# Kernel optimization log

Hardware: AMD Instinct MI355X
Metric: run time of the kernel (lower is better)

## Reference

```python
import jax, jax.numpy as jnp
from jax import lax
import numpy as np

B, ENC, H, DE, T = 16384, 512, 256, 32, 64


def setup_inputs() -> dict:
    key = jax.random.key(0)
    ks = jax.random.split(key, 12)
    s = lambda fan: 1.0 / np.sqrt(fan)
    return {
        "encoded_input_series": jax.random.normal(ks[0], (B, ENC), jnp.float32),
        "final_x_val": jax.random.normal(ks[1], (B, 1), jnp.float32),
        # embed_func: Dense(DE) applied to scalar input (last dim = 1)
        "W_emb": jax.random.normal(ks[2], (1, DE), jnp.float32) * s(1),
        "b_emb": jnp.zeros((DE,), jnp.float32),
        # encode_reshape layer: Dense(H) on encoded series -> initial h
        "W_enc": jax.random.normal(ks[3], (ENC, H), jnp.float32) * s(ENC),
        "b_enc": jnp.zeros((H,), jnp.float32),
        # LSTM cell params (Keras gate order i, f, c, o)
        "W_k": jax.random.normal(ks[4], (DE, 4 * H), jnp.float32) * s(DE),
        "W_r": jax.random.normal(ks[5], (H, 4 * H), jnp.float32) * s(H),
        "b_lstm": jnp.concatenate([jnp.zeros((H,)), jnp.ones((H,)), jnp.zeros((2 * H,))]).astype(jnp.float32),
        # reduce layer: Dense(1)
        "W_red": jax.random.normal(ks[6], (H, 1), jnp.float32) * s(H),
        "b_red": jnp.zeros((1,), jnp.float32),
        "decode_length": T,
    }


def reference(encoded_input_series, final_x_val, W_emb, b_emb, W_enc, b_enc,
              W_k, W_r, b_lstm, W_red, b_red, decode_length):
    Hdim = W_r.shape[0]
    # initial hidden state from encoder summary; cell state zero-initialized
    h0 = encoded_input_series @ W_enc + b_enc            # [B, H]
    c0 = jnp.zeros_like(h0)
    # initial decoder input: embed of last observed value
    x0 = final_x_val @ W_emb + b_emb                     # [B, DE]

    def step(carry, _):
        h, c, x = carry
        gates = x @ W_k + h @ W_r + b_lstm               # [B, 4H]
        i, f, cb, o = jnp.split(gates, 4, axis=-1)
        c_new = jax.nn.sigmoid(f) * c + jax.nn.sigmoid(i) * jnp.tanh(cb)
        h_new = jax.nn.sigmoid(o) * jnp.tanh(c_new)
        y = h_new @ W_red + b_red                        # [B, 1]
        x_next = y @ W_emb + b_emb
        return (h_new, c_new, x_next), y[:, 0]

    _, ys = lax.scan(step, (h0, c0, x0), None, length=decode_length)
    return ys.T                                          # [B, T]
```

## Files before the change

kernel.cpp:

```cpp
#include <hip/hip_runtime.h>
#include <hip/hip_bf16.h>
#include <math.h>


typedef _Float16 f16x8 __attribute__((ext_vector_type(8)));
typedef float f32x4 __attribute__((ext_vector_type(4)));

#define DEV __device__ __forceinline__

constexpr int ENC = 512;
constexpr int HD  = 256;
constexpr int DE  = 32;
constexpr int TT  = 64;
constexpr int NG  = 4 * HD;
constexpr int NKT = 8;
constexpr int TS  = 528;
constexpr int BR  = 32;
constexpr int NMT = 2;

DEV bool is_f32(const void* blstm) {
  return ((const unsigned*)blstm)[256] == 0x3F800000u;
}
DEV float ldf(const void* p, size_t i, bool f32) {
  return f32 ? ((const float*)p)[i]
             : __bfloat162float(((const __hip_bfloat16*)p)[i]);
}
DEV void split2h(float v, _Float16& hi, _Float16& lo) {
  hi = (_Float16)v;
  lo = (_Float16)(v - (float)hi);
}
DEV void ld8cvt2h(const void* p, size_t i, bool f32, f16x8& hi, f16x8& lo) {
  if (f32) {
    const f32x4* q = (const f32x4*)((const float*)p + i);
    f32x4 u0 = q[0], u1 = q[1];
#pragma unroll
    for (int j = 0; j < 4; ++j) {
      float a = u0[j], b = u1[j];
      _Float16 ah = (_Float16)a, bh = (_Float16)b;
      hi[j] = ah; hi[4 + j] = bh;
      lo[j] = (_Float16)(a - (float)ah); lo[4 + j] = (_Float16)(b - (float)bh);
    }
  } else {
    const __hip_bfloat16* s = (const __hip_bfloat16*)p + i;
#pragma unroll
    for (int j = 0; j < 8; ++j) {
      float a = __bfloat162float(s[j]);
      _Float16 ah = (_Float16)a;
      hi[j] = ah;
      lo[j] = (_Float16)(a - (float)ah);
    }
  }
}
DEV f16x8 load8h(const _Float16* p) {
  return *reinterpret_cast<const f16x8*>(p);
}

constexpr float L2E = 1.44269504088896f;
DEV float sigm(float x) {
  return __builtin_amdgcn_rcpf(1.0f + __builtin_amdgcn_exp2f(-L2E * x));
}
DEV float tanh_(float x) {
  return 2.0f * __builtin_amdgcn_rcpf(1.0f + __builtin_amdgcn_exp2f(-2.0f * L2E * x)) - 1.0f;
}

__global__ __launch_bounds__(256) void pack_w(const void* __restrict__ wr,
                                              const void* __restrict__ bl,
                                              _Float16* __restrict__ dhi) {
  const bool f32 = is_f32(bl);
  int idx = blockIdx.x * 256 + threadIdx.x;
  if (idx >= NKT * 64 * 64) return;
  int lane = idx & 63, tile = idx >> 6;
  int nt = tile & 63, ks = tile >> 6;
  int kb = ks * 32 + ((lane >> 4) << 3);
  int n  = (nt << 4) + (lane & 15);
#pragma unroll
  for (int j = 0; j < 8; ++j)
    dhi[idx * 8 + j] = (_Float16)ldf(wr, (size_t)(kb + j) * NG + n, f32);
}

__global__ __launch_bounds__(256) void pack_e(const void* __restrict__ we,
                                              const void* __restrict__ bl,
                                              _Float16* __restrict__ dhi,
                                              _Float16* __restrict__ dlo) {
  const bool f32 = is_f32(bl);
  int idx = blockIdx.x * 256 + threadIdx.x;
  if (idx >= 16 * 16 * 64) return;
  int lane = idx & 63, tile = idx >> 6;
  int nt = tile & 15, ks = tile >> 4;
  int kb = ks * 32 + ((lane >> 4) << 3);
  int n  = (nt << 4) + (lane & 15);
#pragma unroll
  for (int j = 0; j < 8; ++j) {
    float v = ldf(we, (size_t)(kb + j) * HD + n, f32);
    _Float16 h, l;
    split2h(v, h, l);
    dhi[idx * 8 + j] = h;
    dlo[idx * 8 + j] = l;
  }
}

__global__ __launch_bounds__(256) void pack_vec(const void* __restrict__ wemb,
                                                const void* __restrict__ bemb,
                                                const void* __restrict__ wk,
                                                const void* __restrict__ bl,
                                                float* __restrict__ wk2,
                                                float* __restrict__ bp) {
  const bool f32 = is_f32(bl);
  int n = blockIdx.x * 256 + threadIdx.x;
  if (n >= NG) return;
  float s1 = 0.f, s2 = 0.f;
  for (int j = 0; j < DE; ++j) {
    float wkv = ldf(wk, (size_t)j * NG + n, f32);
    s1 += ldf(wemb, j, f32) * wkv;
    s2 += ldf(bemb, j, f32) * wkv;
  }
  wk2[n] = s1;
  bp[n]  = s2 + ldf(bl, n, f32);
}

__global__ __launch_bounds__(512)
__attribute__((amdgpu_waves_per_eu(4, 4)))
void lstm_main(
    const void* __restrict__ enc,
    const void* __restrict__ fx,
    const void* __restrict__ benc,
    const void* __restrict__ blstm,
    const void* __restrict__ wred,
    const void* __restrict__ bredp,
    const _Float16* __restrict__ pWhi,
    const _Float16* __restrict__ pEhi,
    const _Float16* __restrict__ pElo,
    const float* __restrict__ wk2,
    const float* __restrict__ bp,
    const int* __restrict__ dlen,
    void* __restrict__ out) {
  __shared__ __align__(16) _Float16 frag[2][NMT * NKT * TS];
  __shared__ __align__(16) float wredf[HD];
  __shared__ __align__(16) float bpL[NG];
  __shared__ __align__(16) float wk2L[NG];
  __shared__ __align__(16) float y_lds[BR];

  const bool f32 = is_f32(blstm);
  const int tid  = threadIdx.x;
  const int w    = tid >> 6;
  const int lane = tid & 63;
  const int q    = lane >> 4;
  const int cl   = lane & 15;
  const int r0   = blockIdx.x * BR;
  int Tn = dlen[0];
  if (Tn < 1 || Tn > TT) Tn = TT;

  const int aoff = lane * 8;
  const int hwb = w * TS + q * 32 + 128 * (cl >> 3) + (cl & 7);
  const int cbase = w * 32 + cl;

  const int yrow  = tid >> 4, ypart = tid & 15;
  const int ybase = ((yrow >> 4) * NKT + (ypart >> 1)) * TS +
                    ((yrow & 15) + 16 * ((ypart & 1) * 2)) * 8;

  if (tid < HD) wredf[tid] = ldf(wred, tid, f32);
  if (tid < BR) y_lds[tid] = ldf(fx, r0 + tid, f32);
  bpL[tid]        = bp[tid];
  bpL[tid + 512]  = bp[tid + 512];
  wk2L[tid]       = wk2[tid];
  wk2L[tid + 512] = wk2[tid + 512];
  const float bredf = ldf(bredp, 0, f32);

  f32x4 acc0[NMT][2];
  {
    float be0 = ldf(benc, w * 32 + cl, f32);
    float be1 = ldf(benc, w * 32 + 16 + cl, f32);
#pragma unroll
    for (int mt = 0; mt < NMT; ++mt) {
      acc0[mt][0] = (f32x4){be0, be0, be0, be0};
      acc0[mt][1] = (f32x4){be1, be1, be1, be1};
    }
  }
  const size_t ebase = ((size_t)(w * 2) * 64 + lane) * 8;
#pragma unroll 1
  for (int ks = 0; ks < ENC / 32; ++ks) {
    f16x8 bh[2], bl2[2];
#pragma unroll
    for (int hh = 0; hh < 2; ++hh) {
      size_t fo = ebase + (size_t)(ks * 16 + hh) * 512;
      bh[hh]  = load8h(pEhi + fo);
      bl2[hh] = load8h(pElo + fo);
    }
#pragma unroll
    for (int mt = 0; mt < NMT; ++mt) {
      f16x8 ah, al;
      ld8cvt2h(enc, (size_t)(r0 + mt * 16 + cl) * ENC + ks * 32 + q * 8, f32, ah, al);
#pragma unroll
      for (int hh = 0; hh < 2; ++hh) {
        acc0[mt][hh] = __builtin_amdgcn_mfma_f32_16x16x32_f16(ah, bh[hh],  acc0[mt][hh], 0, 0, 0);
        acc0[mt][hh] = __builtin_amdgcn_mfma_f32_16x16x32_f16(al, bh[hh],  acc0[mt][hh], 0, 0, 0);
        acc0[mt][hh] = __builtin_amdgcn_mfma_f32_16x16x32_f16(ah, bl2[hh], acc0[mt][hh], 0, 0, 0);
      }
    }
  }
#pragma unroll
  for (int mt = 0; mt < NMT; ++mt)
#pragma unroll
    for (int hh = 0; hh < 2; ++hh)
#pragma unroll
      for (int r = 0; r < 4; ++r) {
        int idx = mt * NKT * TS + hwb + r * 8 + hh * 256;
        frag[0][idx] = (_Float16)acc0[mt][hh][r];
      }

  f32x4 cst[NMT][2];
#pragma unroll
  for (int mt = 0; mt < NMT; ++mt)
#pragma unroll
    for (int hh = 0; hh < 2; ++hh) cst[mt][hh] = (f32x4){0.f, 0.f, 0.f, 0.f};

  __syncthreads();

  const _Float16* wbase = pWhi + ((size_t)(w * 2) * 64 + lane) * 8;

  int rb = 0;
#pragma unroll 1
  for (int t = 0; t < Tn; ++t) {
    const _Float16* FH = &frag[rb][0];
    _Float16* WH = &frag[rb ^ 1][0];

    f32x4 acc[NMT][8];
#pragma unroll
    for (int nf = 0; nf < 8; ++nf) {
      int col = (nf >> 1) * 256 + (nf & 1) * 16 + cbase;
      float bb = bpL[col];
#pragma unroll
      for (int mt = 0; mt < NMT; ++mt) acc[mt][nf] = (f32x4){bb, bb, bb, bb};
    }

#pragma unroll 1
    for (int j = 0; j < 8; ++j) {
      int ks = (j + w) & 7;
#pragma unroll
      for (int half = 0; half < 2; ++half) {
        f16x8 bc[4];
#pragma unroll
        for (int p = 0; p < 4; ++p)
          bc[p] = load8h(wbase +
                         (size_t)(ks * 64 + (half * 2 + (p >> 1)) * 16 + (p & 1)) * 512);
#pragma unroll
        for (int mt = 0; mt < NMT; ++mt) {
          f16x8 ah = load8h(&FH[(mt * NKT + ks) * TS + aoff]);
#pragma unroll
          for (int p = 0; p < 4; ++p)
            acc[mt][half * 4 + p] =
                __builtin_amdgcn_mfma_f32_16x16x32_f16(ah, bc[p], acc[mt][half * 4 + p], 0, 0, 0);
        }
      }
    }

    if (t > 0) {
      float sum = 0.f;
#pragma unroll
      for (int jj = 0; jj < 2; ++jj) {
        f16x8 hv = load8h(&FH[ybase + jj * 128]);
#pragma unroll
        for (int j = 0; j < 8; ++j)
          sum += (float)hv[j] * wredf[ypart * 16 + jj * 8 + j];
      }
      sum += __shfl_xor(sum, 1);
      sum += __shfl_xor(sum, 2);
      sum += __shfl_xor(sum, 4);
      sum += __shfl_xor(sum, 8);
      float y = sum + bredf;
      if (ypart == 0) {
        size_t oi = (size_t)(r0 + yrow) * TT + (t - 1);
        if (f32) ((float*)out)[oi] = y;
        else     ((__hip_bfloat16*)out)[oi] = __float2bfloat16(y);
        y_lds[yrow] = y;
      }
    }
    __syncthreads();

    f32x4 yv[NMT];
#pragma unroll
    for (int mt = 0; mt < NMT; ++mt)
      yv[mt] = *(const f32x4*)&y_lds[mt * 16 + q * 4];
#pragma unroll
    for (int nf = 0; nf < 8; ++nf) {
      int col = (nf >> 1) * 256 + (nf & 1) * 16 + cbase;
      float wv = wk2L[col];
#pragma unroll
      for (int mt = 0; mt < NMT; ++mt)
#pragma unroll
        for (int r = 0; r < 4; ++r) acc[mt][nf][r] += yv[mt][r] * wv;
    }
#pragma unroll
    for (int mt = 0; mt < NMT; ++mt)
#pragma unroll
      for (int hh = 0; hh < 2; ++hh)
#pragma unroll
        for (int r = 0; r < 4; ++r) {
          float gi = acc[mt][0 + hh][r];
          float gf = acc[mt][2 + hh][r];
          float gc = acc[mt][4 + hh][r];
          float go = acc[mt][6 + hh][r];
          float cn = sigm(gf) * cst[mt][hh][r] + sigm(gi) * tanh_(gc);
          cst[mt][hh][r] = cn;
          float hn = sigm(go) * tanh_(cn);
          int idx = mt * NKT * TS + hwb + r * 8 + hh * 256;
          WH[idx] = (_Float16)hn;
        }
    __syncthreads();
    rb ^= 1;
  }

  {
    const _Float16* FH = &frag[rb][0];
    float sum = 0.f;
#pragma unroll
    for (int jj = 0; jj < 2; ++jj) {
      f16x8 hv = load8h(&FH[ybase + jj * 128]);
#pragma unroll
      for (int j = 0; j < 8; ++j)
        sum += (float)hv[j] * wredf[ypart * 16 + jj * 8 + j];
    }
    sum += __shfl_xor(sum, 1);
    sum += __shfl_xor(sum, 2);
    sum += __shfl_xor(sum, 4);
    sum += __shfl_xor(sum, 8);
    float y = sum + bredf;
    if (ypart == 0) {
      size_t oi = (size_t)(r0 + yrow) * TT + (Tn - 1);
      if (f32) ((float*)out)[oi] = y;
      else     ((__hip_bfloat16*)out)[oi] = __float2bfloat16(y);
    }
  }
}

extern "C" void kernel_launch(void* const* d_in, const int* in_sizes, int n_in,
                              void* d_out, int out_size, void* d_ws, size_t ws_size,
                              hipStream_t stream) {
  const void* enc  = d_in[0];
  const void* fx   = d_in[1];
  const void* wemb = d_in[2];
  const void* bemb = d_in[3];
  const void* wenc = d_in[4];
  const void* benc = d_in[5];
  const void* wk   = d_in[6];
  const void* wr   = d_in[7];
  const void* bl   = d_in[8];
  const void* wred = d_in[9];
  const void* bred = d_in[10];
  const int* dlen  = (const int*)d_in[11];

  _Float16* pWhi = (_Float16*)d_ws;
  _Float16* pEhi = pWhi + NKT * 64 * 64 * 8;
  _Float16* pElo = pEhi + 16 * 16 * 64 * 8;
  float* wk2 = (float*)(pElo + 16 * 16 * 64 * 8);
  float* bp  = wk2 + NG;

  pack_w<<<128, 256, 0, stream>>>(wr, bl, pWhi);
  pack_e<<<64, 256, 0, stream>>>(wenc, bl, pEhi, pElo);
  pack_vec<<<4, 256, 0, stream>>>(wemb, bemb, wk, bl, wk2, bp);

  int nblocks = in_sizes[1] / BR;
  lstm_main<<<nblocks, 512, 0, stream>>>(enc, fx, benc, bl, wred, bred,
                                         pWhi, pEhi, pElo, wk2, bp, dlen, d_out);
}
```

Before: 943.9 us.

## Fold autoregressive feedback into recurrent weights to drop per-step barrier

Folds the linear feedback path (y = h·W_red + b_red, x = y·W_emb + b_emb, x·W_k) into a modified recurrent weight matrix W_r + W_red⊗wk2 and an adjusted bias. Step 0 still uses the original weights plus the final_x_val term. This removes the y_lds round trip, one __syncthreads per timestep and the per-step rank-1 update, so the output reduction no longer sits on the critical path. The cost is a second packed fp16 weight copy and extra rounding error, because the folded weights are stored in fp16.

```diff
diff --git a/kernel.cpp b/kernel.cpp
--- a/kernel.cpp
+++ b/kernel.cpp
@@ -63,9 +63,35 @@
   return 2.0f * __builtin_amdgcn_rcpf(1.0f + __builtin_amdgcn_exp2f(-2.0f * L2E * x)) - 1.0f;
 }
 
+__global__ __launch_bounds__(256) void pack_vec(const void* __restrict__ wemb,
+                                                const void* __restrict__ bemb,
+                                                const void* __restrict__ wk,
+                                                const void* __restrict__ bl,
+                                                const void* __restrict__ bredp,
+                                                float* __restrict__ wk2,
+                                                float* __restrict__ bp,
+                                                float* __restrict__ bp2) {
+  const bool f32 = is_f32(bl);
+  int n = blockIdx.x * 256 + threadIdx.x;
+  if (n >= NG) return;
+  float s1 = 0.f, s2 = 0.f;
+  for (int j = 0; j < DE; ++j) {
+    float wkv = ldf(wk, (size_t)j * NG + n, f32);
+    s1 += ldf(wemb, j, f32) * wkv;
+    s2 += ldf(bemb, j, f32) * wkv;
+  }
+  float b = s2 + ldf(bl, n, f32);
+  wk2[n] = s1;
+  bp[n]  = b;
+  bp2[n] = b + ldf(bredp, 0, f32) * s1;
+}
+
 __global__ __launch_bounds__(256) void pack_w(const void* __restrict__ wr,
                                               const void* __restrict__ bl,
-                                              _Float16* __restrict__ dhi) {
+                                              const void* __restrict__ wred,
+                                              const float* __restrict__ wk2,
+                                              _Float16* __restrict__ d0,
+                                              _Float16* __restrict__ d1) {
   const bool f32 = is_f32(bl);
   int idx = blockIdx.x * 256 + threadIdx.x;
   if (idx >= NKT * 64 * 64) return;
@@ -73,9 +99,14 @@
   int nt = tile & 63, ks = tile >> 6;
   int kb = ks * 32 + ((lane >> 4) << 3);
   int n  = (nt << 4) + (lane & 15);
-#pragma unroll
-  for (int j = 0; j < 8; ++j)
-    dhi[idx * 8 + j] = (_Float16)ldf(wr, (size_t)(kb + j) * NG + n, f32);
+  float wn = wk2[n];
+#pragma unroll
+  for (int j = 0; j < 8; ++j) {
+    int k = kb + j;
+    float v = ldf(wr, (size_t)k * NG + n, f32);
+    d0[idx * 8 + j] = (_Float16)v;
+    d1[idx * 8 + j] = (_Float16)(v + ldf(wred, k, f32) * wn);
+  }
 }
 
 __global__ __launch_bounds__(256) void pack_e(const void* __restrict__ we,
@@ -99,25 +130,6 @@
   }
 }
 
-__global__ __launch_bounds__(256) void pack_vec(const void* __restrict__ wemb,
-                                                const void* __restrict__ bemb,
-                                                const void* __restrict__ wk,
-                                                const void* __restrict__ bl,
-                                                float* __restrict__ wk2,
-                                                float* __restrict__ bp) {
-  const bool f32 = is_f32(bl);
-  int n = blockIdx.x * 256 + threadIdx.x;
-  if (n >= NG) return;
-  float s1 = 0.f, s2 = 0.f;
-  for (int j = 0; j < DE; ++j) {
-    float wkv = ldf(wk, (size_t)j * NG + n, f32);
-    s1 += ldf(wemb, j, f32) * wkv;
-    s2 += ldf(bemb, j, f32) * wkv;
-  }
-  wk2[n] = s1;
-  bp[n]  = s2 + ldf(bl, n, f32);
-}
-
 __global__ __launch_bounds__(512)
 __attribute__((amdgpu_waves_per_eu(4, 4)))
 void lstm_main(
@@ -127,18 +139,21 @@
     const void* __restrict__ blstm,
     const void* __restrict__ wred,
     const void* __restrict__ bredp,
-    const _Float16* __restrict__ pWhi,
+    const _Float16* __restrict__ pW0,
+    const _Float16* __restrict__ pW1,
     const _Float16* __restrict__ pEhi,
     const _Float16* __restrict__ pElo,
     const float* __restrict__ wk2,
     const float* __restrict__ bp,
+    const float* __restrict__ bp2,
     const int* __restrict__ dlen,
     void* __restrict__ out) {
   __shared__ __align__(16) _Float16 frag[2][NMT * NKT * TS];
   __shared__ __align__(16) float wredf[HD];
-  __shared__ __align__(16) float bpL[NG];
+  __shared__ __align__(16) float bp0L[NG];
+  __shared__ __align__(16) float bp2L[NG];
   __shared__ __align__(16) float wk2L[NG];
-  __shared__ __align__(16) float y_lds[BR];
+  __shared__ __align__(16) float fxL[BR];
 
   const bool f32 = is_f32(blstm);
   const int tid  = threadIdx.x;
@@ -159,11 +174,13 @@
                     ((yrow & 15) + 16 * ((ypart & 1) * 2)) * 8;
 
   if (tid < HD) wredf[tid] = ldf(wred, tid, f32);
-  if (tid < BR) y_lds[tid] = ldf(fx, r0 + tid, f32);
-  bpL[tid]        = bp[tid];
-  bpL[tid + 512]  = bp[tid + 512];
-  wk2L[tid]       = wk2[tid];
-  wk2L[tid + 512] = wk2[tid + 512];
+  if (tid < BR) fxL[tid] = ldf(fx, r0 + tid, f32);
+  bp0L[tid]        = bp[tid];
+  bp0L[tid + 512]  = bp[tid + 512];
+  bp2L[tid]        = bp2[tid];
+  bp2L[tid + 512]  = bp2[tid + 512];
+  wk2L[tid]        = wk2[tid];
+  wk2L[tid + 512]  = wk2[tid + 512];
   const float bredf = ldf(bredp, 0, f32);
 
   f32x4 acc0[NMT][2];
@@ -216,7 +233,8 @@
 
   __syncthreads();
 
-  const _Float16* wbase = pWhi + ((size_t)(w * 2) * 64 + lane) * 8;
+  const _Float16* wbase0 = pW0 + ((size_t)(w * 2) * 64 + lane) * 8;
+  const _Float16* wbase1 = pW1 + ((size_t)(w * 2) * 64 + lane) * 8;
 
   int rb = 0;
 #pragma unroll 1
@@ -225,14 +243,34 @@
     _Float16* WH = &frag[rb ^ 1][0];
 
     f32x4 acc[NMT][8];
-#pragma unroll
-    for (int nf = 0; nf < 8; ++nf) {
-      int col = (nf >> 1) * 256 + (nf & 1) * 16 + cbase;
-      float bb = bpL[col];
-#pragma unroll
-      for (int mt = 0; mt < NMT; ++mt) acc[mt][nf] = (f32x4){bb, bb, bb, bb};
-    }
-
+    if (t == 0) {
+      f32x4 fxv[NMT];
+#pragma unroll
+      for (int mt = 0; mt < NMT; ++mt)
+        fxv[mt] = *(const f32x4*)&fxL[mt * 16 + q * 4];
+#pragma unroll
+      for (int nf = 0; nf < 8; ++nf) {
+        int col = (nf >> 1) * 256 + (nf & 1) * 16 + cbase;
+        float bb = bp0L[col], wv = wk2L[col];
+#pragma unroll
+        for (int mt = 0; mt < NMT; ++mt) {
+          f32x4 a;
+#pragma unroll
+          for (int r = 0; r < 4; ++r) a[r] = bb + fxv[mt][r] * wv;
+          acc[mt][nf] = a;
+        }
+      }
+    } else {
+#pragma unroll
+      for (int nf = 0; nf < 8; ++nf) {
+        int col = (nf >> 1) * 256 + (nf & 1) * 16 + cbase;
+        float bb = bp2L[col];
+#pragma unroll
+        for (int mt = 0; mt < NMT; ++mt) acc[mt][nf] = (f32x4){bb, bb, bb, bb};
+      }
+    }
+
+    const _Float16* wb = (t == 0) ? wbase0 : wbase1;
 #pragma unroll 1
     for (int j = 0; j < 8; ++j) {
       int ks = (j + w) & 7;
@@ -241,7 +279,7 @@
         f16x8 bc[4];
 #pragma unroll
         for (int p = 0; p < 4; ++p)
-          bc[p] = load8h(wbase +
+          bc[p] = load8h(wb +
                          (size_t)(ks * 64 + (half * 2 + (p >> 1)) * 16 + (p & 1)) * 512);
 #pragma unroll
         for (int mt = 0; mt < NMT; ++mt) {
@@ -267,29 +305,14 @@
       sum += __shfl_xor(sum, 2);
       sum += __shfl_xor(sum, 4);
       sum += __shfl_xor(sum, 8);
-      float y = sum + bredf;
       if (ypart == 0) {
+        float y = sum + bredf;
         size_t oi = (size_t)(r0 + yrow) * TT + (t - 1);
         if (f32) ((float*)out)[oi] = y;
         else     ((__hip_bfloat16*)out)[oi] = __float2bfloat16(y);
-        y_lds[yrow] = y;
-      }
-    }
-    __syncthreads();
-
-    f32x4 yv[NMT];
-#pragma unroll
-    for (int mt = 0; mt < NMT; ++mt)
-      yv[mt] = *(const f32x4*)&y_lds[mt * 16 + q * 4];
-#pragma unroll
-    for (int nf = 0; nf < 8; ++nf) {
-      int col = (nf >> 1) * 256 + (nf & 1) * 16 + cbase;
-      float wv = wk2L[col];
-#pragma unroll
-      for (int mt = 0; mt < NMT; ++mt)
-#pragma unroll
-        for (int r = 0; r < 4; ++r) acc[mt][nf][r] += yv[mt][r] * wv;
-    }
+      }
+    }
+
 #pragma unroll
     for (int mt = 0; mt < NMT; ++mt)
 #pragma unroll
@@ -324,8 +347,8 @@
     sum += __shfl_xor(sum, 2);
     sum += __shfl_xor(sum, 4);
     sum += __shfl_xor(sum, 8);
-    float y = sum + bredf;
     if (ypart == 0) {
+      float y = sum + bredf;
       size_t oi = (size_t)(r0 + yrow) * TT + (Tn - 1);
       if (f32) ((float*)out)[oi] = y;
       else     ((__hip_bfloat16*)out)[oi] = __float2bfloat16(y);
@@ -349,17 +372,20 @@
   const void* bred = d_in[10];
   const int* dlen  = (const int*)d_in[11];
 
-  _Float16* pWhi = (_Float16*)d_ws;
-  _Float16* pEhi = pWhi + NKT * 64 * 64 * 8;
+  _Float16* pW0 = (_Float16*)d_ws;
+  _Float16* pW1 = pW0 + NKT * 64 * 64 * 8;
+  _Float16* pEhi = pW1 + NKT * 64 * 64 * 8;
   _Float16* pElo = pEhi + 16 * 16 * 64 * 8;
   float* wk2 = (float*)(pElo + 16 * 16 * 64 * 8);
   float* bp  = wk2 + NG;
-
-  pack_w<<<128, 256, 0, stream>>>(wr, bl, pWhi);
+  float* bp2 = bp + NG;
+
+  pack_vec<<<4, 256, 0, stream>>>(wemb, bemb, wk, bl, bred, wk2, bp, bp2);
+  pack_w<<<128, 256, 0, stream>>>(wr, bl, wred, wk2, pW0, pW1);
   pack_e<<<64, 256, 0, stream>>>(wenc, bl, pEhi, pElo);
-  pack_vec<<<4, 256, 0, stream>>>(wemb, bemb, wk, bl, wk2, bp);
 
   int nblocks = in_sizes[1] / BR;
   lstm_main<<<nblocks, 512, 0, stream>>>(enc, fx, benc, bl, wred, bred,
-                                         pWhi, pEhi, pElo, wk2, bp, dlen, d_out);
-}
+                                         pW0, pW1, pEhi, pElo, wk2, bp, bp2,
+                                         dlen, d_out);
+}
```

Result: no change. 941.8 us (-0.2%).
